# Performance work log

Measured on AMD Instinct MI355X. Metric: run time of the kernel, lower is better.

## Reference

```python
import jax, jax.numpy as jnp
import numpy as np

B, S, D = 8, 2048, 128

def setup_inputs() -> dict:
    key = jax.random.key(0)
    kq, kk, kv, km = jax.random.split(key, 4)
    q = jax.random.normal(kq, (B, S, D), dtype=jnp.float32)
    k = jax.random.normal(kk, (B, S, D), dtype=jnp.float32)
    v = jax.random.normal(kv, (B, S, D), dtype=jnp.float32)
    mask = jax.random.randint(km, (B, S), 0, 2).astype(bool)  # True = masked out
    return {"q": q, "k": k, "v": v, "mask": mask}

def reference(q, k, v, mask):
    scaler = np.sqrt(D).astype(np.float32)
    # score[b, i, j] = <q_i, k_j> / sqrt(d_k)
    score = jnp.einsum('bik,bjk->bij', q, k) / scaler
    score = score - jnp.max(score, axis=-1, keepdims=True)
    e = jnp.exp(score)
    # mask is (B, S_kv): broadcast across query positions, zero out masked keys
    e = jnp.where(mask[:, None, :], 0.0, e)
    a = e / jnp.sum(e, axis=-1, keepdims=True)
    c = jnp.einsum('bij,bjd->bid', a, v)
    return c
```

## Files before the change

kernel.cpp:

```cpp
#include <hip/hip_runtime.h>
#include <hip/hip_fp16.h>
#include <math.h>

typedef __attribute__((ext_vector_type(8))) short short8;
typedef __attribute__((ext_vector_type(16))) float floatx16;
typedef __attribute__((ext_vector_type(2))) __bf16 bf16x2;
typedef __attribute__((ext_vector_type(2))) unsigned int uint2v;

namespace {
constexpr int Bn = 8;
constexpr int Sn = 2048;
constexpr int Dn = 128;
constexpr int BQ = 128;
constexpr int BK = 64;
constexpr int QTILES = Sn / BQ;
constexpr int NKB = Sn / BK;
constexpr int ROWS = Bn * Sn;
constexpr int NSPLIT = 4;
constexpr float SC2 = 0.12753102063642597f;
constexpr float DEFER_THR = 8.0f;
constexpr int TILE_USH = BK * Dn;
}

#if __has_builtin(__builtin_amdgcn_exp2f)
#define EXP2(x) __builtin_amdgcn_exp2f(x)
#else
#define EXP2(x) exp2f(x)
#endif

__device__ __forceinline__ unsigned short f2bf(float x) {
  union { float f; unsigned u; } a; a.f = x;
  unsigned r = a.u + 0x7fffu + ((a.u >> 16) & 1u);
  return (unsigned short)(r >> 16);
}

__device__ __forceinline__ unsigned pack2bf(float x, float y) {
  union { bf16x2 b; unsigned u; } c;
  c.b[0] = (__bf16)x; c.b[1] = (__bf16)y;
  return c.u;
}

__device__ __forceinline__ uint2v pl32swap(unsigned a, unsigned b, int h) {
#if __has_builtin(__builtin_amdgcn_permlane32_swap)
  (void)h;
  return __builtin_amdgcn_permlane32_swap(a, b, false, false);
#else
  unsigned ax = __shfl_xor((int)a, 32);
  unsigned bx = __shfl_xor((int)b, 32);
  uint2v r;
  r[0] = h ? bx : a;
  r[1] = h ? b : ax;
  return r;
#endif
}

__device__ __forceinline__ void gl_lds16(const void* g, void* l, int lane) {
#if __has_builtin(__builtin_amdgcn_global_load_lds)
  (void)lane;
  __builtin_amdgcn_global_load_lds((const __attribute__((address_space(1))) unsigned int*)g,
                                   (__attribute__((address_space(3))) unsigned int*)l, 16, 0, 0);
#else
  *(float4*)((char*)l + lane * 16) = *(const float4*)g;
#endif
}

__global__ __launch_bounds__(256)
void mask_scan(const unsigned char* __restrict__ mraw,
               unsigned short* __restrict__ idxg, int* __restrict__ cntg) {
  __shared__ int sc[256];
  const int b = blockIdx.x;
  const int t = threadIdx.x;

  unsigned wv = ((const unsigned int*)mraw)[t];
  int any1  = __syncthreads_or((wv & 0x0000ff00u) ? 1 : 0);
  int any23 = __syncthreads_or((wv & 0xffff0000u) ? 1 : 0);
  const int mlayout = any1 ? 1 : (any23 ? 2 : 0);

  const int s0 = t * 8;
  const int gbase = b * Sn + s0;
  bool ms[8];
  if (mlayout == 1) {
    #pragma unroll
    for (int i = 0; i < 8; ++i) ms[i] = mraw[gbase + i] != 0;
  } else if (mlayout == 2) {
    const float* mf = (const float*)mraw;
    #pragma unroll
    for (int i = 0; i < 8; ++i) ms[i] = mf[gbase + i] != 0.0f;
  } else {
    const int* mi = (const int*)mraw;
    #pragma unroll
    for (int i = 0; i < 8; ++i) ms[i] = mi[gbase + i] != 0;
  }

  int c = 0;
  #pragma unroll
  for (int i = 0; i < 8; ++i) c += ms[i] ? 0 : 1;
  sc[t] = c;
  __syncthreads();
  for (int off = 1; off < 256; off <<= 1) {
    int v = (t >= off) ? sc[t - off] : 0;
    __syncthreads();
    sc[t] += v;
    __syncthreads();
  }
  const int incl = sc[t];
  const int total = sc[255];
  int pos = incl - c;
  #pragma unroll
  for (int i = 0; i < 8; ++i)
    if (!ms[i]) idxg[b * Sn + (pos++)] = (unsigned short)(s0 + i);
  if (t == 0) cntg[b] = total;
}

__global__ __launch_bounds__(256)
void prep(const float* __restrict__ kg, const float* __restrict__ vg,
          const unsigned short* __restrict__ idxg, const int* __restrict__ cntg,
          unsigned short* __restrict__ Kpg, unsigned short* __restrict__ Vpg) {
  __shared__ __align__(16) float Vf[16 * 136];
  const int p = blockIdx.x;
  const int b = p >> 7, qq = p & 127;
  const int kb = qq >> 2, k16 = qq & 3;
  const int t = threadIdx.x;

  const int cnt = cntg[b];
  const int padded = (cnt + 63) & ~63;
  const int slot0 = kb * 64 + k16 * 16;
  if (slot0 >= padded) return;

  const int j  = t >> 4;
  const int o8 = t & 15;
  const int sl = slot0 + j;
  const bool real = sl < cnt;

  float4 a, bq, va, vb;
  if (real) {
    const int srow = idxg[b * Sn + sl];
    const size_t base = ((size_t)(b * Sn + srow)) * 32 + o8 * 2;
    a  = ((const float4*)kg)[base]; bq = ((const float4*)kg)[base + 1];
    va = ((const float4*)vg)[base]; vb = ((const float4*)vg)[base + 1];
  } else {
    a = bq = va = vb = make_float4(0.f, 0.f, 0.f, 0.f);
  }

  {
    union { unsigned u[4]; short8 s8; } pk;
    pk.u[0] = pack2bf(a.x, a.y);   pk.u[1] = pack2bf(a.z, a.w);
    pk.u[2] = pack2bf(bq.x, bq.y); pk.u[3] = pack2bf(bq.z, bq.w);
    const int jl = k16 * 16 + j;
    *(short8*)(Kpg + (size_t)(b * NKB + kb) * TILE_USH + jl * 128 + ((o8 ^ (jl & 7)) * 8)) = pk.s8;
  }
  {
    *(float4*)&Vf[j * 136 + o8 * 8]     = va;
    *(float4*)&Vf[j * 136 + o8 * 8 + 4] = vb;
  }
  __syncthreads();
  {
    const int d = t >> 1, h = t & 1;
    union { unsigned u[4]; short8 s8; } pv;
    #pragma unroll
    for (int i = 0; i < 4; ++i)
      pv.u[i] = pack2bf(Vf[(h * 8 + 2 * i) * 136 + d], Vf[(h * 8 + 2 * i + 1) * 136 + d]);
    const int og = k16 * 2 + h;
    *(short8*)(Vpg + (size_t)(b * NKB + kb) * TILE_USH + d * 64 + ((og ^ (d & 7)) * 8)) = pv.s8;
  }
}


__device__ __forceinline__ void stage_tile(const char* gsrc, char* ldst,
                                           int stagebase, int L) {
  #pragma unroll
  for (int i = 0; i < 4; ++i) {
    const int off = stagebase + i * 1024;
    gl_lds16(gsrc + off + L * 16, ldst + off, L);
  }
}

__device__ __forceinline__ void qk_tile(const unsigned short* __restrict__ Kc,
                                        int q, int h, int sw,
                                        const short8 (&qh)[8], const short8 (&ql)[8],
                                        floatx16 (&s)[2]) {
  #pragma unroll
  for (int kg = 0; kg < 2; ++kg)
    #pragma unroll
    for (int r = 0; r < 16; ++r) s[kg][r] = 0.0f;
  #pragma unroll
  for (int kstep = 0; kstep < 8; ++kstep) {
    const int ko = ((kstep * 2 + h) ^ sw) * 8;
    #pragma unroll
    for (int kg = 0; kg < 2; ++kg) {
      short8 kf = *(const short8*)&Kc[(kg * 32 + q) * 128 + ko];
      s[kg] = __builtin_amdgcn_mfma_f32_32x32x16_bf16(kf, qh[kstep], s[kg], 0, 0, 0);
      s[kg] = __builtin_amdgcn_mfma_f32_32x32x16_bf16(kf, ql[kstep], s[kg], 0, 0, 0);
    }
  }
}

__device__ __forceinline__ void tile_body(
    int kbc, int kbN,
    const unsigned short* __restrict__ Kread, unsigned short* Kdst,
    const unsigned short* __restrict__ Vread, unsigned short* Vdst,
    const char* ktile, const char* vtile, int stagebase, int L,
    int cnt,
    int q, int h, int sw,
    const short8 (&qh)[8], const short8 (&ql)[8],
    floatx16 (&sCur)[2], floatx16 (&sNxt)[2],
    floatx16 (&O32)[4], float& m_i, float& l_i, float& mtrue) {
  __syncthreads();

  if (kbc + 2 < kbN)
    stage_tile(ktile + (size_t)(kbc + 2) * (TILE_USH * 2), (char*)Kdst, stagebase, L);
  const bool hasNext = (kbc + 1 < kbN);
  if (hasNext)
    stage_tile(vtile + (size_t)(kbc + 1) * (TILE_USH * 2), (char*)Vdst, stagebase, L);

  if (hasNext)
    qk_tile(Kread, q, h, sw, qh, ql, sNxt);

  if ((kbc + 1) * BK <= cnt) {
    #pragma unroll
    for (int kg = 0; kg < 2; ++kg)
      #pragma unroll
      for (int r = 0; r < 16; ++r) sCur[kg][r] *= SC2;
  } else {
    #pragma unroll
    for (int kg = 0; kg < 2; ++kg)
      #pragma unroll
      for (int r = 0; r < 16; ++r) {
        const int key = kbc * BK + kg * 32 + ((r & 3) + 8 * (r >> 2)) + 4 * h;
        sCur[kg][r] = fmaf(sCur[kg][r], SC2, (key < cnt) ? 0.0f : -1e30f);
      }
  }
  float mxp[4] = {-INFINITY, -INFINITY, -INFINITY, -INFINITY};
  #pragma unroll
  for (int kg = 0; kg < 2; ++kg)
    #pragma unroll
    for (int r = 0; r < 16; ++r) mxp[r & 3] = fmaxf(mxp[r & 3], sCur[kg][r]);
  float mx = fmaxf(fmaxf(mxp[0], mxp[1]), fmaxf(mxp[2], mxp[3]));
  mx = fmaxf(mx, __shfl_xor(mx, 32));
  mtrue = fmaxf(mtrue, mx);

  float mnew;
  if (__all(mx <= m_i + DEFER_THR)) {
    mnew = m_i;
  } else {
    mnew = fmaxf(m_i, mx);
    const float alpha = EXP2(m_i - mnew);
    l_i *= alpha;
    #pragma unroll
    for (int dg = 0; dg < 4; ++dg)
      #pragma unroll
      for (int r = 0; r < 16; ++r) O32[dg][r] *= alpha;
  }

  float rsp[4] = {0.f, 0.f, 0.f, 0.f};
  #pragma unroll
  for (int kg = 0; kg < 2; ++kg)
    #pragma unroll
    for (int r = 0; r < 16; ++r) {
      float e = EXP2(sCur[kg][r] - mnew);
      sCur[kg][r] = e;
      rsp[r & 3] += e;
    }
  float rs = (rsp[0] + rsp[1]) + (rsp[2] + rsp[3]);
  rs += __shfl_xor(rs, 32);
  l_i += rs;
  m_i = mnew;

  unsigned xw[2][4][2];
  #pragma unroll
  for (int kg = 0; kg < 2; ++kg)
    #pragma unroll
    for (int m = 0; m < 4; ++m) {
      xw[kg][m][0] = pack2bf(sCur[kg][4 * m + 0], sCur[kg][4 * m + 1]);
      xw[kg][m][1] = pack2bf(sCur[kg][4 * m + 2], sCur[kg][4 * m + 3]);
    }
  unsigned pfw[4][4];
  #pragma unroll
  for (int kg = 0; kg < 2; ++kg)
    #pragma unroll
    for (int j = 0; j < 2; ++j)
      #pragma unroll
      for (int c2 = 0; c2 < 2; ++c2) {
        uint2v r = pl32swap(xw[kg][2 * j][c2], xw[kg][2 * j + 1][c2], h);
        pfw[kg * 2 + j][c2]     = r[0];
        pfw[kg * 2 + j][2 + c2] = r[1];
      }

  __builtin_amdgcn_s_setprio(1);
  #pragma unroll
  for (int k2 = 0; k2 < 4; ++k2) {
    const int ko = ((k2 * 2 + h) ^ sw) * 8;
    union { unsigned u[4]; short8 s8; } pw;
    pw.u[0] = pfw[k2][0]; pw.u[1] = pfw[k2][1];
    pw.u[2] = pfw[k2][2]; pw.u[3] = pfw[k2][3];
    #pragma unroll
    for (int dg = 0; dg < 4; ++dg) {
      short8 vf = *(const short8*)&Vread[(dg * 32 + q) * 64 + ko];
      O32[dg] = __builtin_amdgcn_mfma_f32_32x32x16_bf16(vf, pw.s8, O32[dg], 0, 0, 0);
    }
  }
  __builtin_amdgcn_s_setprio(0);
}

template<int SPLIT, bool DIRECT>
__global__ __launch_bounds__(256, 2)
void attn_fwd(const float* __restrict__ qg,
              const unsigned short* __restrict__ Kpg,
              const unsigned short* __restrict__ Vpg,
              const int* __restrict__ cntg,
              float* __restrict__ outg, __half* __restrict__ Op,
              float* __restrict__ Mp, float* __restrict__ Lp) {
  __shared__ __align__(16) unsigned short Khi[2][TILE_USH];
  __shared__ __align__(16) unsigned short Vt[2][TILE_USH];

  const int tid = threadIdx.x;
  const int bid = blockIdx.x;
  const int b   = bid & 7;
  const int q0  = ((bid >> 3) & (QTILES - 1)) * BQ;
  const int s   = bid >> 7;
  const int w   = tid >> 6;
  const int L   = tid & 63;
  const int q   = L & 31;
  const int h   = L >> 5;
  const int sw  = q & 7;

  const int cnt = cntg[b];
  const int nt  = (cnt + 63) >> 6;
  const int kb0 = (s * nt) / SPLIT;
  const int kbN = ((s + 1) * nt) / SPLIT;
  const int T   = kbN - kb0;

  const int row = b * Sn + q0 + w * 32 + q;

  if (T <= 0) {
    if constexpr (DIRECT) {
      float* orow = outg + (size_t)row * Dn;
      float4 z = make_float4(0.f, 0.f, 0.f, 0.f);
      #pragma unroll
      for (int dg = 0; dg < 4; ++dg)
        #pragma unroll
        for (int ro = 0; ro < 4; ++ro) *(float4*)&orow[dg * 32 + 8 * ro + 4 * h] = z;
    } else {
      __half* orow = Op + ((size_t)s * ROWS + row) * Dn;
      uint2 z; z.x = 0u; z.y = 0u;
      #pragma unroll
      for (int dg = 0; dg < 4; ++dg)
        #pragma unroll
        for (int ro = 0; ro < 4; ++ro) *(uint2*)&orow[dg * 32 + 8 * ro + 4 * h] = z;
      if (h == 0) { Mp[s * ROWS + row] = -INFINITY; Lp[s * ROWS + row] = 0.0f; }
    }
    return;
  }

  const char* ktile = (const char*)(Kpg + (size_t)b * NKB * TILE_USH);
  const char* vtile = (const char*)(Vpg + (size_t)b * NKB * TILE_USH);
  const int stagebase = w * 4096;

  short8 qh[8], ql[8];
  {
    const float* qrow = qg + (size_t)row * Dn;
    #pragma unroll
    for (int kstep = 0; kstep < 8; ++kstep) {
      float4 f0 = *(const float4*)(qrow + kstep * 16 + h * 8);
      float4 f1 = *(const float4*)(qrow + kstep * 16 + h * 8 + 4);
      float xs[8] = {f0.x, f0.y, f0.z, f0.w, f1.x, f1.y, f1.z, f1.w};
      #pragma unroll
      for (int j = 0; j < 8; ++j) {
        unsigned short hi = f2bf(xs[j]);
        union { unsigned u; float f; } hv; hv.u = ((unsigned)hi) << 16;
        qh[kstep][j] = (short)hi;
        ql[kstep][j] = (short)f2bf(xs[j] - hv.f);
      }
    }
  }

  float m_i = -INFINITY, l_i = 0.0f;
  float mtrue = -INFINITY;
  floatx16 O32[4];
  #pragma unroll
  for (int dg = 0; dg < 4; ++dg)
    #pragma unroll
    for (int r = 0; r < 16; ++r) O32[dg][r] = 0.0f;

  stage_tile(ktile + (size_t)kb0 * (TILE_USH * 2), (char*)Khi[0], stagebase, L);
  stage_tile(vtile + (size_t)kb0 * (TILE_USH * 2), (char*)Vt[0], stagebase, L);
  __syncthreads();
  if (kb0 + 1 < kbN)
    stage_tile(ktile + (size_t)(kb0 + 1) * (TILE_USH * 2), (char*)Khi[1], stagebase, L);

  floatx16 sA[2], sB[2];
  qk_tile(Khi[0], q, h, sw, qh, ql, sA);

  int kb = kb0;
  for (; kb + 2 <= kbN; kb += 2) {
    tile_body(kb, kbN, Khi[1], Khi[0], Vt[0], Vt[1], ktile, vtile, stagebase, L,
              cnt, q, h, sw, qh, ql, sA, sB, O32, m_i, l_i, mtrue);
    tile_body(kb + 1, kbN, Khi[0], Khi[1], Vt[1], Vt[0], ktile, vtile, stagebase, L,
              cnt, q, h, sw, qh, ql, sB, sA, O32, m_i, l_i, mtrue);
  }
  if (kb < kbN)
    tile_body(kb, kbN, Khi[1], Khi[0], Vt[0], Vt[1], ktile, vtile, stagebase, L,
              cnt, q, h, sw, qh, ql, sA, sB, O32, m_i, l_i, mtrue);

  if constexpr (DIRECT) {
    const float inv = 1.0f / l_i;
    float* orow = outg + (size_t)row * Dn;
    #pragma unroll
    for (int dg = 0; dg < 4; ++dg)
      #pragma unroll
      for (int ro = 0; ro < 4; ++ro) {
        float4 f = make_float4(O32[dg][4 * ro] * inv,     O32[dg][4 * ro + 1] * inv,
                               O32[dg][4 * ro + 2] * inv, O32[dg][4 * ro + 3] * inv);
        *(float4*)&orow[dg * 32 + 8 * ro + 4 * h] = f;
      }
  } else {
    const float fin = EXP2(m_i - mtrue);
    __half* orow = Op + ((size_t)s * ROWS + row) * Dn;
    #pragma unroll
    for (int dg = 0; dg < 4; ++dg)
      #pragma unroll
      for (int ro = 0; ro < 4; ++ro) {
        union { __half2 h2[2]; uint2 u; } pk;
        pk.h2[0] = __floats2half2_rn(O32[dg][4 * ro] * fin,     O32[dg][4 * ro + 1] * fin);
        pk.h2[1] = __floats2half2_rn(O32[dg][4 * ro + 2] * fin, O32[dg][4 * ro + 3] * fin);
        *(uint2*)&orow[dg * 32 + 8 * ro + 4 * h] = pk.u;
      }
    if (h == 0) {
      Mp[s * ROWS + row] = mtrue;
      Lp[s * ROWS + row] = l_i * fin;
    }
  }
}

__global__ __launch_bounds__(256)
void attn_combine(const __half* __restrict__ Op, const float* __restrict__ Mp,
                  const float* __restrict__ Lp, float4* __restrict__ out4) {
  const int gid = blockIdx.x * 256 + threadIdx.x;
  const int row = gid >> 5;
  const int c4  = gid & 31;
  float ms[NSPLIT];
  float m = -INFINITY;
  #pragma unroll
  for (int s = 0; s < NSPLIT; ++s) { ms[s] = Mp[s * ROWS + row]; m = fmaxf(m, ms[s]); }
  float l = 0.0f;
  float4 acc = make_float4(0.f, 0.f, 0.f, 0.f);
  #pragma unroll
  for (int s = 0; s < NSPLIT; ++s) {
    float wgt = EXP2(ms[s] - m);
    l = fmaf(Lp[s * ROWS + row], wgt, l);
    union { uint2 u; __half2 h2[2]; } pk;
    pk.u = ((const uint2*)Op)[(size_t)(s * ROWS + row) * 32 + c4];
    float2 f0 = __half22float2(pk.h2[0]);
    float2 f1 = __half22float2(pk.h2[1]);
    acc.x = fmaf(f0.x, wgt, acc.x);
    acc.y = fmaf(f0.y, wgt, acc.y);
    acc.z = fmaf(f1.x, wgt, acc.z);
    acc.w = fmaf(f1.y, wgt, acc.w);
  }
  float inv = 1.0f / l;
  out4[(size_t)row * 32 + c4] = make_float4(acc.x * inv, acc.y * inv, acc.z * inv, acc.w * inv);
}

extern "C" void kernel_launch(void* const* d_in, const int* in_sizes, int n_in,
                              void* d_out, int out_size, void* d_ws, size_t ws_size,
                              hipStream_t stream) {
  const float* q = (const float*)d_in[0];
  const float* k = (const float*)d_in[1];
  const float* v = (const float*)d_in[2];
  const unsigned char* m = (const unsigned char*)d_in[3];
  float* out = (float*)d_out;
  (void)in_sizes; (void)n_in; (void)out_size;

  constexpr size_t OPB = (size_t)NSPLIT * ROWS * Dn * sizeof(__half);
  constexpr size_t MLB = (size_t)NSPLIT * ROWS * sizeof(float);
  constexpr size_t KPB = (size_t)Bn * NKB * TILE_USH * 2;
  constexpr size_t CNTB = 64;
  constexpr size_t IDXB = (size_t)Bn * Sn * sizeof(unsigned short);

  char* ws = (char*)d_ws;
  if (ws_size >= OPB + 2 * MLB + 2 * KPB + CNTB + IDXB) {
    __half* Op = (__half*)ws;
    float* Mp = (float*)(ws + OPB);
    float* Lp = (float*)(ws + OPB + MLB);
    unsigned short* Kp = (unsigned short*)(ws + OPB + 2 * MLB);
    unsigned short* Vp = (unsigned short*)(ws + OPB + 2 * MLB + KPB);
    int* cnt = (int*)(ws + OPB + 2 * MLB + 2 * KPB);
    unsigned short* idx = (unsigned short*)(ws + OPB + 2 * MLB + 2 * KPB + CNTB);
    mask_scan<<<dim3(Bn), dim3(256), 0, stream>>>(m, idx, cnt);
    prep<<<dim3(Bn * NKB * 4), dim3(256), 0, stream>>>(k, v, idx, cnt, Kp, Vp);
    attn_fwd<NSPLIT, false><<<dim3(Bn * QTILES * NSPLIT), dim3(256), 0, stream>>>(
        q, Kp, Vp, cnt, out, Op, Mp, Lp);
    attn_combine<<<dim3(ROWS * 32 / 256), dim3(256), 0, stream>>>(
        Op, Mp, Lp, (float4*)out);
  } else if (ws_size >= 2 * KPB + CNTB + IDXB) {
    unsigned short* Kp = (unsigned short*)ws;
    unsigned short* Vp = (unsigned short*)(ws + KPB);
    int* cnt = (int*)(ws + 2 * KPB);
    unsigned short* idx = (unsigned short*)(ws + 2 * KPB + CNTB);
    mask_scan<<<dim3(Bn), dim3(256), 0, stream>>>(m, idx, cnt);
    prep<<<dim3(Bn * NKB * 4), dim3(256), 0, stream>>>(k, v, idx, cnt, Kp, Vp);
    attn_fwd<1, true><<<dim3(Bn * QTILES), dim3(256), 0, stream>>>(
        q, Kp, Vp, cnt, out, nullptr, nullptr, nullptr);
  }
}
```

Baseline: 120.8 us.

## Read K/V tiles directly from global memory instead of LDS double-buffering

Removes the shared-memory staging of K and V tiles (global_load_lds double buffering with barriers and the software-pipelined QK of the next tile) and replaces it with a simple loop that reads packed K/V fragments straight from global memory for each tile. This drops the barriers and LDS traffic and frees LDS, which may allow more resident blocks. In exchange, every wave loads K/V itself through the cache hierarchy with no explicit prefetch, so load latency is exposed and reuse across the four waves depends on L1/L2 hits.

After: 110.2 us. 1.1x faster.

```diff
diff --git a/kernel.cpp b/kernel.cpp
--- a/kernel.cpp
+++ b/kernel.cpp
@@ -54,16 +54,6 @@
 #endif
 }
 
-__device__ __forceinline__ void gl_lds16(const void* g, void* l, int lane) {
-#if __has_builtin(__builtin_amdgcn_global_load_lds)
-  (void)lane;
-  __builtin_amdgcn_global_load_lds((const __attribute__((address_space(1))) unsigned int*)g,
-                                   (__attribute__((address_space(3))) unsigned int*)l, 16, 0, 0);
-#else
-  *(float4*)((char*)l + lane * 16) = *(const float4*)g;
-#endif
-}
-
 __global__ __launch_bounds__(256)
 void mask_scan(const unsigned char* __restrict__ mraw,
                unsigned short* __restrict__ idxg, int* __restrict__ cntg) {
@@ -165,143 +155,6 @@
   }
 }
 
-
-__device__ __forceinline__ void stage_tile(const char* gsrc, char* ldst,
-                                           int stagebase, int L) {
-  #pragma unroll
-  for (int i = 0; i < 4; ++i) {
-    const int off = stagebase + i * 1024;
-    gl_lds16(gsrc + off + L * 16, ldst + off, L);
-  }
-}
-
-__device__ __forceinline__ void qk_tile(const unsigned short* __restrict__ Kc,
-                                        int q, int h, int sw,
-                                        const short8 (&qh)[8], const short8 (&ql)[8],
-                                        floatx16 (&s)[2]) {
-  #pragma unroll
-  for (int kg = 0; kg < 2; ++kg)
-    #pragma unroll
-    for (int r = 0; r < 16; ++r) s[kg][r] = 0.0f;
-  #pragma unroll
-  for (int kstep = 0; kstep < 8; ++kstep) {
-    const int ko = ((kstep * 2 + h) ^ sw) * 8;
-    #pragma unroll
-    for (int kg = 0; kg < 2; ++kg) {
-      short8 kf = *(const short8*)&Kc[(kg * 32 + q) * 128 + ko];
-      s[kg] = __builtin_amdgcn_mfma_f32_32x32x16_bf16(kf, qh[kstep], s[kg], 0, 0, 0);
-      s[kg] = __builtin_amdgcn_mfma_f32_32x32x16_bf16(kf, ql[kstep], s[kg], 0, 0, 0);
-    }
-  }
-}
-
-__device__ __forceinline__ void tile_body(
-    int kbc, int kbN,
-    const unsigned short* __restrict__ Kread, unsigned short* Kdst,
-    const unsigned short* __restrict__ Vread, unsigned short* Vdst,
-    const char* ktile, const char* vtile, int stagebase, int L,
-    int cnt,
-    int q, int h, int sw,
-    const short8 (&qh)[8], const short8 (&ql)[8],
-    floatx16 (&sCur)[2], floatx16 (&sNxt)[2],
-    floatx16 (&O32)[4], float& m_i, float& l_i, float& mtrue) {
-  __syncthreads();
-
-  if (kbc + 2 < kbN)
-    stage_tile(ktile + (size_t)(kbc + 2) * (TILE_USH * 2), (char*)Kdst, stagebase, L);
-  const bool hasNext = (kbc + 1 < kbN);
-  if (hasNext)
-    stage_tile(vtile + (size_t)(kbc + 1) * (TILE_USH * 2), (char*)Vdst, stagebase, L);
-
-  if (hasNext)
-    qk_tile(Kread, q, h, sw, qh, ql, sNxt);
-
-  if ((kbc + 1) * BK <= cnt) {
-    #pragma unroll
-    for (int kg = 0; kg < 2; ++kg)
-      #pragma unroll
-      for (int r = 0; r < 16; ++r) sCur[kg][r] *= SC2;
-  } else {
-    #pragma unroll
-    for (int kg = 0; kg < 2; ++kg)
-      #pragma unroll
-      for (int r = 0; r < 16; ++r) {
-        const int key = kbc * BK + kg * 32 + ((r & 3) + 8 * (r >> 2)) + 4 * h;
-        sCur[kg][r] = fmaf(sCur[kg][r], SC2, (key < cnt) ? 0.0f : -1e30f);
-      }
-  }
-  float mxp[4] = {-INFINITY, -INFINITY, -INFINITY, -INFINITY};
-  #pragma unroll
-  for (int kg = 0; kg < 2; ++kg)
-    #pragma unroll
-    for (int r = 0; r < 16; ++r) mxp[r & 3] = fmaxf(mxp[r & 3], sCur[kg][r]);
-  float mx = fmaxf(fmaxf(mxp[0], mxp[1]), fmaxf(mxp[2], mxp[3]));
-  mx = fmaxf(mx, __shfl_xor(mx, 32));
-  mtrue = fmaxf(mtrue, mx);
-
-  float mnew;
-  if (__all(mx <= m_i + DEFER_THR)) {
-    mnew = m_i;
-  } else {
-    mnew = fmaxf(m_i, mx);
-    const float alpha = EXP2(m_i - mnew);
-    l_i *= alpha;
-    #pragma unroll
-    for (int dg = 0; dg < 4; ++dg)
-      #pragma unroll
-      for (int r = 0; r < 16; ++r) O32[dg][r] *= alpha;
-  }
-
-  float rsp[4] = {0.f, 0.f, 0.f, 0.f};
-  #pragma unroll
-  for (int kg = 0; kg < 2; ++kg)
-    #pragma unroll
-    for (int r = 0; r < 16; ++r) {
-      float e = EXP2(sCur[kg][r] - mnew);
-      sCur[kg][r] = e;
-      rsp[r & 3] += e;
-    }
-  float rs = (rsp[0] + rsp[1]) + (rsp[2] + rsp[3]);
-  rs += __shfl_xor(rs, 32);
-  l_i += rs;
-  m_i = mnew;
-
-  unsigned xw[2][4][2];
-  #pragma unroll
-  for (int kg = 0; kg < 2; ++kg)
-    #pragma unroll
-    for (int m = 0; m < 4; ++m) {
-      xw[kg][m][0] = pack2bf(sCur[kg][4 * m + 0], sCur[kg][4 * m + 1]);
-      xw[kg][m][1] = pack2bf(sCur[kg][4 * m + 2], sCur[kg][4 * m + 3]);
-    }
-  unsigned pfw[4][4];
-  #pragma unroll
-  for (int kg = 0; kg < 2; ++kg)
-    #pragma unroll
-    for (int j = 0; j < 2; ++j)
-      #pragma unroll
-      for (int c2 = 0; c2 < 2; ++c2) {
-        uint2v r = pl32swap(xw[kg][2 * j][c2], xw[kg][2 * j + 1][c2], h);
-        pfw[kg * 2 + j][c2]     = r[0];
-        pfw[kg * 2 + j][2 + c2] = r[1];
-      }
-
-  __builtin_amdgcn_s_setprio(1);
-  #pragma unroll
-  for (int k2 = 0; k2 < 4; ++k2) {
-    const int ko = ((k2 * 2 + h) ^ sw) * 8;
-    union { unsigned u[4]; short8 s8; } pw;
-    pw.u[0] = pfw[k2][0]; pw.u[1] = pfw[k2][1];
-    pw.u[2] = pfw[k2][2]; pw.u[3] = pfw[k2][3];
-    #pragma unroll
-    for (int dg = 0; dg < 4; ++dg) {
-      short8 vf = *(const short8*)&Vread[(dg * 32 + q) * 64 + ko];
-      O32[dg] = __builtin_amdgcn_mfma_f32_32x32x16_bf16(vf, pw.s8, O32[dg], 0, 0, 0);
-    }
-  }
-  __builtin_amdgcn_s_setprio(0);
-}
-
 template<int SPLIT, bool DIRECT>
 __global__ __launch_bounds__(256, 2)
 void attn_fwd(const float* __restrict__ qg,
@@ -310,9 +163,6 @@
               const int* __restrict__ cntg,
               float* __restrict__ outg, __half* __restrict__ Op,
               float* __restrict__ Mp, float* __restrict__ Lp) {
-  __shared__ __align__(16) unsigned short Khi[2][TILE_USH];
-  __shared__ __align__(16) unsigned short Vt[2][TILE_USH];
-
   const int tid = threadIdx.x;
   const int bid = blockIdx.x;
   const int b   = bid & 7;
@@ -352,9 +202,8 @@
     return;
   }
 
-  const char* ktile = (const char*)(Kpg + (size_t)b * NKB * TILE_USH);
-  const char* vtile = (const char*)(Vpg + (size_t)b * NKB * TILE_USH);
-  const int stagebase = w * 4096;
+  const unsigned short* ktile = Kpg + (size_t)b * NKB * TILE_USH;
+  const unsigned short* vtile = Vpg + (size_t)b * NKB * TILE_USH;
 
   short8 qh[8], ql[8];
   {
@@ -382,25 +231,110 @@
     #pragma unroll
     for (int r = 0; r < 16; ++r) O32[dg][r] = 0.0f;
 
-  stage_tile(ktile + (size_t)kb0 * (TILE_USH * 2), (char*)Khi[0], stagebase, L);
-  stage_tile(vtile + (size_t)kb0 * (TILE_USH * 2), (char*)Vt[0], stagebase, L);
-  __syncthreads();
-  if (kb0 + 1 < kbN)
-    stage_tile(ktile + (size_t)(kb0 + 1) * (TILE_USH * 2), (char*)Khi[1], stagebase, L);
-
-  floatx16 sA[2], sB[2];
-  qk_tile(Khi[0], q, h, sw, qh, ql, sA);
-
-  int kb = kb0;
-  for (; kb + 2 <= kbN; kb += 2) {
-    tile_body(kb, kbN, Khi[1], Khi[0], Vt[0], Vt[1], ktile, vtile, stagebase, L,
-              cnt, q, h, sw, qh, ql, sA, sB, O32, m_i, l_i, mtrue);
-    tile_body(kb + 1, kbN, Khi[0], Khi[1], Vt[1], Vt[0], ktile, vtile, stagebase, L,
-              cnt, q, h, sw, qh, ql, sB, sA, O32, m_i, l_i, mtrue);
-  }
-  if (kb < kbN)
-    tile_body(kb, kbN, Khi[1], Khi[0], Vt[0], Vt[1], ktile, vtile, stagebase, L,
-              cnt, q, h, sw, qh, ql, sA, sB, O32, m_i, l_i, mtrue);
+  for (int kb = kb0; kb < kbN; ++kb) {
+    const unsigned short* Kc = ktile + (size_t)kb * TILE_USH;
+    const unsigned short* Vc = vtile + (size_t)kb * TILE_USH;
+
+    floatx16 sS[2];
+    #pragma unroll
+    for (int kg = 0; kg < 2; ++kg)
+      #pragma unroll
+      for (int r = 0; r < 16; ++r) sS[kg][r] = 0.0f;
+    #pragma unroll
+    for (int kstep = 0; kstep < 8; ++kstep) {
+      const int ko = ((kstep * 2 + h) ^ sw) * 8;
+      #pragma unroll
+      for (int kg = 0; kg < 2; ++kg) {
+        short8 kf = *(const short8*)&Kc[(kg * 32 + q) * 128 + ko];
+        sS[kg] = __builtin_amdgcn_mfma_f32_32x32x16_bf16(kf, qh[kstep], sS[kg], 0, 0, 0);
+        sS[kg] = __builtin_amdgcn_mfma_f32_32x32x16_bf16(kf, ql[kstep], sS[kg], 0, 0, 0);
+      }
+    }
+
+    if ((kb + 1) * BK <= cnt) {
+      #pragma unroll
+      for (int kg = 0; kg < 2; ++kg)
+        #pragma unroll
+        for (int r = 0; r < 16; ++r) sS[kg][r] *= SC2;
+    } else {
+      #pragma unroll
+      for (int kg = 0; kg < 2; ++kg)
+        #pragma unroll
+        for (int r = 0; r < 16; ++r) {
+          const int key = kb * BK + kg * 32 + ((r & 3) + 8 * (r >> 2)) + 4 * h;
+          sS[kg] = sS[kg];
+          sS[kg][r] = fmaf(sS[kg][r], SC2, (key < cnt) ? 0.0f : -1e30f);
+        }
+    }
+    float mxp[4] = {-INFINITY, -INFINITY, -INFINITY, -INFINITY};
+    #pragma unroll
+    for (int kg = 0; kg < 2; ++kg)
+      #pragma unroll
+      for (int r = 0; r < 16; ++r) mxp[r & 3] = fmaxf(mxp[r & 3], sS[kg][r]);
+    float mx = fmaxf(fmaxf(mxp[0], mxp[1]), fmaxf(mxp[2], mxp[3]));
+    mx = fmaxf(mx, __shfl_xor(mx, 32));
+    mtrue = fmaxf(mtrue, mx);
+
+    float mnew;
+    if (__all(mx <= m_i + DEFER_THR)) {
+      mnew = m_i;
+    } else {
+      mnew = fmaxf(m_i, mx);
+      const float alpha = EXP2(m_i - mnew);
+      l_i *= alpha;
+      #pragma unroll
+      for (int dg = 0; dg < 4; ++dg)
+        #pragma unroll
+        for (int r = 0; r < 16; ++r) O32[dg][r] *= alpha;
+    }
+
+    float rsp[4] = {0.f, 0.f, 0.f, 0.f};
+    #pragma unroll
+    for (int kg = 0; kg < 2; ++kg)
+      #pragma unroll
+      for (int r = 0; r < 16; ++r) {
+        float e = EXP2(sS[kg][r] - mnew);
+        sS[kg][r] = e;
+        rsp[r & 3] += e;
+      }
+    float rs = (rsp[0] + rsp[1]) + (rsp[2] + rsp[3]);
+    rs += __shfl_xor(rs, 32);
+    l_i += rs;
+    m_i = mnew;
+
+    unsigned xw[2][4][2];
+    #pragma unroll
+    for (int kg = 0; kg < 2; ++kg)
+      #pragma unroll
+      for (int m = 0; m < 4; ++m) {
+        xw[kg][m][0] = pack2bf(sS[kg][4 * m + 0], sS[kg][4 * m + 1]);
+        xw[kg][m][1] = pack2bf(sS[kg][4 * m + 2], sS[kg][4 * m + 3]);
+      }
+    unsigned pfw[4][4];
+    #pragma unroll
+    for (int kg = 0; kg < 2; ++kg)
+      #pragma unroll
+      for (int j = 0; j < 2; ++j)
+        #pragma unroll
+        for (int c2 = 0; c2 < 2; ++c2) {
+          uint2v r = pl32swap(xw[kg][2 * j][c2], xw[kg][2 * j + 1][c2], h);
+          pfw[kg * 2 + j][c2]     = r[0];
+          pfw[kg * 2 + j][2 + c2] = r[1];
+        }
+
+    #pragma unroll
+    for (int k2 = 0; k2 < 4; ++k2) {
+      const int ko = ((k2 * 2 + h) ^ sw) * 8;
+      union { unsigned u[4]; short8 s8; } pw;
+      pw.u[0] = pfw[k2][0]; pw.u[1] = pfw[k2][1];
+      pw.u[2] = pfw[k2][2]; pw.u[3] = pfw[k2][3];
+      #pragma unroll
+      for (int dg = 0; dg < 4; ++dg) {
+        short8 vf = *(const short8*)&Vc[(dg * 32 + q) * 64 + ko];
+        O32[dg] = __builtin_amdgcn_mfma_f32_32x32x16_bf16(vf, pw.s8, O32[dg], 0, 0, 0);
+      }
+    }
+  }
 
   if constexpr (DIRECT) {
     const float inv = 1.0f / l_i;
```
